# Kernel tuning notes

Hardware: AMD Instinct MI355X
Metric: run time of the kernel (lower is better)

## Reference

```python
import jax, jax.numpy as jnp
import numpy as np

B_POINTS = 2097152
N_LEVELS = 16
BASE_RES = 16.0
PER_LEVEL_SCALE = 1.3195079565048218
MAX_PARAMS = 2 ** 19
PRIMES = np.array([1, 2654435761, 805459861], dtype=np.uint32)
# corner bit pattern: idx in [0,8), dim d offset = (idx >> d) & 1
CORNER_BITS = np.array([[(idx >> d) & 1 for d in range(3)] for idx in range(8)], dtype=np.uint32)  # (8,3)


def _level_meta():
    offsets, sizes, indicators = [], [], []
    off = 0
    for i in range(N_LEVELS):
        res = int(np.ceil(BASE_RES * np.exp(i * np.log(PER_LEVEL_SCALE)) - 1.0)) + 1
        p = res ** 3
        p = p if p % 8 == 0 else ((p + 7) // 8) * 8
        p = min(MAX_PARAMS, p)
        offsets.append(off)
        sizes.append(p)
        indicators.append(1 if res ** 3 <= p else 0)
        off += p
    return offsets, sizes, indicators, off

OFFSETS, MAP_SIZES, INDICATORS, TOTAL_HASH = _level_meta()
TOTAL_PARAMS = TOTAL_HASH * 2  # 2 features per entry, interleaved


def setup_inputs() -> dict:
    key = jax.random.key(0)
    k1, k2 = jax.random.split(key)
    positions = jax.random.uniform(k1, (B_POINTS, 3), dtype=jnp.float32)
    # matches random_initialize: uniform in (-1e-4, 1e-4)
    table = (jax.random.uniform(k2, (TOTAL_PARAMS,), dtype=jnp.float32) * 2.0 - 1.0) * 1e-4
    return {"positions": positions, "table": table}


def _encode(positions, table):
    outs = []
    frac_bits = CORNER_BITS.astype(np.float32)[None, :, :]  # (1,8,3)
    for level in range(N_LEVELS):
        scale = np.float32(BASE_RES * np.exp(level * np.log(PER_LEVEL_SCALE)) - 1.0)
        resolution = np.uint32(np.ceil(scale)) + np.uint32(1)
        pos = positions * scale + 0.5                       # (B,3)
        pos_floor = jnp.floor(pos)
        frac = pos - pos_floor                              # (B,3)
        pg = pos_floor.astype(jnp.uint32)                   # (B,3)
        coords = pg[:, None, :] + CORNER_BITS[None, :, :]   # (B,8,3) uint32
        # trilinear weights per corner
        w = jnp.prod(frac[:, None, :] * frac_bits + (1.0 - frac[:, None, :]) * (1.0 - frac_bits), axis=-1)  # (B,8)
        if INDICATORS[level] == 1:
            s1 = resolution
            s2 = resolution * resolution  # uint32 wraparound safe (res small here)
            h = coords[..., 0] + coords[..., 1] * s1 + coords[..., 2] * s2
        else:
            h = (coords[..., 0] * PRIMES[0]) ^ (coords[..., 1] * PRIMES[1]) ^ (coords[..., 2] * PRIMES[2])
        idx = (h % np.uint32(MAP_SIZES[level])).astype(jnp.int32)
        base = OFFSETS[level] * 2 + idx * 2                 # (B,8) int32
        f0 = jnp.take(table, base)                          # (B,8)
        f1 = jnp.take(table, base + 1)
        outs.append(jnp.stack([jnp.sum(w * f0, axis=-1), jnp.sum(w * f1, axis=-1)], axis=-1))  # (B,2)
    return jnp.concatenate(outs, axis=-1)                   # (B,32)


def reference(positions, table):
    return _encode(positions, table)
```

## Files before the change

### kernel.cpp

```cpp
#include <hip/hip_runtime.h>
#include <cmath>

#define NLEV 16
#define TPB 256

typedef float v4f __attribute__((ext_vector_type(4)));
typedef float v2f __attribute__((ext_vector_type(2)));

static constexpr unsigned kRes[NLEV] = {16u,22u,28u,37u,49u,65u,85u,112u,148u,195u,257u,338u,446u,589u,777u,1025u};
static constexpr unsigned kMsz[NLEV] = {4096u,10648u,21952u,50656u,117656u,274632u,
  524288u,524288u,524288u,524288u,524288u,524288u,524288u,524288u,524288u,524288u};
static constexpr unsigned kOff[NLEV] = {0u,4096u,14744u,36696u,87352u,205008u,479640u,1003928u,
  1528216u,2052504u,2576792u,3101080u,3625368u,4149656u,4673944u,5198232u};
static constexpr int kDense[NLEV] = {1,1,1,1,1,1,0,0,0,0,0,0,0,0,0,0};

struct ScaleParams { float s[NLEV]; };


__device__ __forceinline__ void load_pos(const float* __restrict__ pos, float* sp,
                                         int tid, size_t pbase,
                                         float& px, float& py, float& pz) {
  const float* src = pos + pbase * 3;
  sp[tid]       = __builtin_nontemporal_load(src + tid);
  sp[tid + 256] = __builtin_nontemporal_load(src + tid + 256);
  sp[tid + 512] = __builtin_nontemporal_load(src + tid + 512);
  __syncthreads();
  px = sp[tid*3 + 0]; py = sp[tid*3 + 1]; pz = sp[tid*3 + 2];
}

template<int L>
__global__ __launch_bounds__(TPB, 8) void hash_level(
    const float* __restrict__ pos, const float* __restrict__ table,
    float* __restrict__ ws, float scale, int npts)
{
  __shared__ float sp[TPB * 3];
  const int tid = threadIdx.x;
  const size_t pbase = (size_t)blockIdx.x * TPB;
  float px, py, pz;
  load_pos(pos, sp, tid, pbase, px, py, pz);

  const float x = px * scale + 0.5f;
  const float y = py * scale + 0.5f;
  const float z = pz * scale + 0.5f;
  const float xf = floorf(x), yf = floorf(y), zf = floorf(z);
  const float tx = x - xf, ty = y - yf, tz = z - zf;
  const unsigned xi = (unsigned)xf, yi = (unsigned)yf, zi = (unsigned)zf;

  const unsigned hx[2] = {xi, xi + 1u};
  const unsigned hy[2] = {yi * 2654435761u, (yi + 1u) * 2654435761u};
  const unsigned hz[2] = {zi * 805459861u,  (zi + 1u) * 805459861u};
  const float wx[2] = {1.0f - tx, tx};
  const float wy[2] = {1.0f - ty, ty};
  const float wz[2] = {1.0f - tz, tz};

  const float2* __restrict__ tab2 = (const float2*)table;
  float a0 = 0.0f, a1 = 0.0f;
#pragma unroll
  for (int c = 0; c < 8; ++c) {
    const unsigned idx = (hx[c & 1] ^ hy[(c >> 1) & 1] ^ hz[(c >> 2) & 1]) & (kMsz[L] - 1u);
    const float2 f = tab2[kOff[L] + idx];
    const float w = wx[c & 1] * wy[(c >> 1) & 1] * wz[(c >> 2) & 1];
    a0 = fmaf(w, f.x, a0);
    a1 = fmaf(w, f.y, a1);
  }
  v2f r; r.x = a0; r.y = a1;
  __builtin_nontemporal_store(r, (v2f*)ws + (size_t)L * npts + pbase + tid);
}

__global__ __launch_bounds__(TPB, 4) void dense_levels(
    const float* __restrict__ pos, const float* __restrict__ table,
    float* __restrict__ ws, ScaleParams spar, int npts)
{
  __shared__ float sp[TPB * 3];
  const int tid = threadIdx.x;
  const size_t pbase = (size_t)blockIdx.x * TPB;
  float px, py, pz;
  load_pos(pos, sp, tid, pbase, px, py, pz);

  const float2* __restrict__ tab2 = (const float2*)table;
#pragma unroll
  for (int L = 0; L < 6; ++L) {
    const float scale = spar.s[L];
    const float x = px * scale + 0.5f;
    const float y = py * scale + 0.5f;
    const float z = pz * scale + 0.5f;
    const float xf = floorf(x), yf = floorf(y), zf = floorf(z);
    const float tx = x - xf, ty = y - yf, tz = z - zf;
    const unsigned xi = (unsigned)xf, yi = (unsigned)yf, zi = (unsigned)zf;

    const unsigned r = kRes[L];
    const unsigned hx[2] = {xi, xi + 1u};
    const unsigned hy[2] = {yi * r, (yi + 1u) * r};
    const unsigned hz[2] = {zi * r * r, (zi + 1u) * r * r};
    const float wx[2] = {1.0f - tx, tx};
    const float wy[2] = {1.0f - ty, ty};
    const float wz[2] = {1.0f - tz, tz};

    float a0 = 0.0f, a1 = 0.0f;
#pragma unroll
    for (int c = 0; c < 8; ++c) {
      const unsigned h = hx[c & 1] + hy[(c >> 1) & 1] + hz[(c >> 2) & 1];
      const unsigned idx = (h >= kMsz[L]) ? (h - kMsz[L]) : h;
      const float2 f = tab2[kOff[L] + idx];
      const float w = wx[c & 1] * wy[(c >> 1) & 1] * wz[(c >> 2) & 1];
      a0 = fmaf(w, f.x, a0);
      a1 = fmaf(w, f.y, a1);
    }
    v2f rr; rr.x = a0; rr.y = a1;
    __builtin_nontemporal_store(rr, (v2f*)ws + (size_t)L * npts + pbase + tid);
  }
}

__global__ __launch_bounds__(TPB, 4) void transpose_out(
    const float* __restrict__ ws, float* __restrict__ out, int npts)
{
  __shared__ float lds[TPB * 33];
  const int tid = threadIdx.x;
  const size_t pbase = (size_t)blockIdx.x * TPB;
#pragma unroll
  for (int L = 0; L < NLEV; ++L) {
    const v2f w = __builtin_nontemporal_load((const v2f*)ws + (size_t)L * npts + pbase + tid);
    lds[tid * 33 + 2 * L]     = w.x;
    lds[tid * 33 + 2 * L + 1] = w.y;
  }
  __syncthreads();
  v4f* out4 = (v4f*)out + (size_t)blockIdx.x * (TPB * 32 / 4);
#pragma unroll
  for (int k = 0; k < 8; ++k) {
    const int q  = tid + k * TPB;
    const int p  = q >> 3;
    const int c4 = (q & 7) * 4;
    v4f v;
    v.x = lds[p * 33 + c4 + 0];
    v.y = lds[p * 33 + c4 + 1];
    v.z = lds[p * 33 + c4 + 2];
    v.w = lds[p * 33 + c4 + 3];
    __builtin_nontemporal_store(v, out4 + q);
  }
}

__global__ __launch_bounds__(TPB) void hashenc_kernel(
    const float* __restrict__ pos, const float* __restrict__ table,
    float* __restrict__ out, ScaleParams spar)
{
  __shared__ float lds[TPB * 33];
  const int tid = threadIdx.x;
  const size_t pbase = (size_t)blockIdx.x * TPB;
  {
    const float* src = pos + pbase * 3;
    lds[tid]        = src[tid];
    lds[tid + 256]  = src[tid + 256];
    lds[tid + 512]  = src[tid + 512];
  }
  __syncthreads();
  const float px = lds[tid*3 + 0];
  const float py = lds[tid*3 + 1];
  const float pz = lds[tid*3 + 2];
  __syncthreads();

  const float2* __restrict__ tab2 = (const float2*)table;
  float acc[2 * NLEV];

#pragma unroll
  for (int L = 0; L < NLEV; ++L) {
    const float scale = spar.s[L];
    const float x = px * scale + 0.5f;
    const float y = py * scale + 0.5f;
    const float z = pz * scale + 0.5f;
    const float xf = floorf(x), yf = floorf(y), zf = floorf(z);
    const float tx = x - xf, ty = y - yf, tz = z - zf;
    const unsigned xi = (unsigned)xf, yi = (unsigned)yf, zi = (unsigned)zf;

    unsigned hx[2], hy[2], hz[2];
    if (kDense[L]) {
      const unsigned r = kRes[L];
      hx[0] = xi;          hx[1] = xi + 1u;
      hy[0] = yi * r;      hy[1] = (yi + 1u) * r;
      hz[0] = zi * r * r;  hz[1] = (zi + 1u) * r * r;
    } else {
      hx[0] = xi;                 hx[1] = xi + 1u;
      hy[0] = yi * 2654435761u;   hy[1] = (yi + 1u) * 2654435761u;
      hz[0] = zi * 805459861u;    hz[1] = (zi + 1u) * 805459861u;
    }
    const float wx[2] = {1.0f - tx, tx};
    const float wy[2] = {1.0f - ty, ty};
    const float wz[2] = {1.0f - tz, tz};

    float a0 = 0.0f, a1 = 0.0f;
#pragma unroll
    for (int c = 0; c < 8; ++c) {
      unsigned idx;
      if (kDense[L]) {
        unsigned h = hx[c & 1] + hy[(c >> 1) & 1] + hz[(c >> 2) & 1];
        idx = (h >= kMsz[L]) ? (h - kMsz[L]) : h;
      } else {
        idx = (hx[c & 1] ^ hy[(c >> 1) & 1] ^ hz[(c >> 2) & 1]) & (kMsz[L] - 1u);
      }
      const float2 f = tab2[kOff[L] + idx];
      const float w = wx[c & 1] * wy[(c >> 1) & 1] * wz[(c >> 2) & 1];
      a0 = fmaf(w, f.x, a0);
      a1 = fmaf(w, f.y, a1);
    }
    acc[2 * L]     = a0;
    acc[2 * L + 1] = a1;
  }

#pragma unroll
  for (int c = 0; c < 32; ++c) lds[tid * 33 + c] = acc[c];
  __syncthreads();

  v4f* out4 = (v4f*)out + (size_t)blockIdx.x * (TPB * 32 / 4);
#pragma unroll
  for (int k = 0; k < 8; ++k) {
    const int q  = tid + k * TPB;
    const int p  = q >> 3;
    const int c4 = (q & 7) * 4;
    v4f v;
    v.x = lds[p * 33 + c4 + 0];
    v.y = lds[p * 33 + c4 + 1];
    v.z = lds[p * 33 + c4 + 2];
    v.w = lds[p * 33 + c4 + 3];
    __builtin_nontemporal_store(v, out4 + q);
  }
}

extern "C" void kernel_launch(void* const* d_in, const int* in_sizes, int n_in,
                              void* d_out, int out_size, void* d_ws, size_t ws_size,
                              hipStream_t stream) {
  const float* pos   = (const float*)d_in[0];
  const float* table = (const float*)d_in[1];
  float* out = (float*)d_out;

  ScaleParams sp;
  for (int i = 0; i < NLEV; ++i)
    sp.s[i] = (float)(16.0 * exp((double)i * log(1.3195079565048218)) - 1.0);

  const int npts = in_sizes[0] / 3;
  const int nblk = npts / TPB;
  const size_t need = (size_t)npts * 32 * sizeof(float);

  if (ws_size >= need) {
    float* wsf = (float*)d_ws;
    dense_levels<<<nblk, TPB, 0, stream>>>(pos, table, wsf, sp, npts);
    hash_level< 6><<<nblk, TPB, 0, stream>>>(pos, table, wsf, sp.s[ 6], npts);
    hash_level< 7><<<nblk, TPB, 0, stream>>>(pos, table, wsf, sp.s[ 7], npts);
    hash_level< 8><<<nblk, TPB, 0, stream>>>(pos, table, wsf, sp.s[ 8], npts);
    hash_level< 9><<<nblk, TPB, 0, stream>>>(pos, table, wsf, sp.s[ 9], npts);
    hash_level<10><<<nblk, TPB, 0, stream>>>(pos, table, wsf, sp.s[10], npts);
    hash_level<11><<<nblk, TPB, 0, stream>>>(pos, table, wsf, sp.s[11], npts);
    hash_level<12><<<nblk, TPB, 0, stream>>>(pos, table, wsf, sp.s[12], npts);
    hash_level<13><<<nblk, TPB, 0, stream>>>(pos, table, wsf, sp.s[13], npts);
    hash_level<14><<<nblk, TPB, 0, stream>>>(pos, table, wsf, sp.s[14], npts);
    hash_level<15><<<nblk, TPB, 0, stream>>>(pos, table, wsf, sp.s[15], npts);
    transpose_out<<<nblk, TPB, 0, stream>>>(wsf, out, npts);
  } else {
    hashenc_kernel<<<nblk, TPB, 0, stream>>>(pos, table, out, sp);
  }
}
```

Before: 1.069 ms.

## Fuse hash-level launches into one kernel, two points per thread, paired dense loads

The ten per-level hash kernels become a single `hash_fused` launch. Each block derives its level from the high bits of its block index, so blocks stay grouped by level and each level's table slice keeps its cache locality. Both the dense and hash kernels now handle two points per thread and write 16-byte results. The dense levels fetch the two x-adjacent corners with one 16-byte load, patching the single case where the second corner wraps to the start of the level's table. This trades launch overhead and load-instruction count for more registers per thread, and adds a fallback to the old kernel when the point count is not a power-of-two multiple of 512.

Result: slower. 1.112 ms (+4.0%).

```diff
diff --git a/kernel.cpp b/kernel.cpp
--- a/kernel.cpp
+++ b/kernel.cpp
@@ -16,29 +16,30 @@
 
 struct ScaleParams { float s[NLEV]; };
 
-
-__device__ __forceinline__ void load_pos(const float* __restrict__ pos, float* sp,
-                                         int tid, size_t pbase,
-                                         float& px, float& py, float& pz) {
+__device__ __forceinline__ v4f load4_a8(const float* p) {
+  const float* q = (const float*)__builtin_assume_aligned((const void*)p, 8);
+  v4f v;
+  __builtin_memcpy(&v, q, 16);
+  return v;
+}
+
+__device__ __forceinline__ void load_pos2(const float* __restrict__ pos, float* sp,
+                                          int tid, size_t pbase,
+                                          float& px0, float& py0, float& pz0,
+                                          float& px1, float& py1, float& pz1) {
   const float* src = pos + pbase * 3;
-  sp[tid]       = __builtin_nontemporal_load(src + tid);
-  sp[tid + 256] = __builtin_nontemporal_load(src + tid + 256);
-  sp[tid + 512] = __builtin_nontemporal_load(src + tid + 512);
-  __syncthreads();
-  px = sp[tid*3 + 0]; py = sp[tid*3 + 1]; pz = sp[tid*3 + 2];
-}
-
-template<int L>
-__global__ __launch_bounds__(TPB, 8) void hash_level(
-    const float* __restrict__ pos, const float* __restrict__ table,
-    float* __restrict__ ws, float scale, int npts)
-{
-  __shared__ float sp[TPB * 3];
-  const int tid = threadIdx.x;
-  const size_t pbase = (size_t)blockIdx.x * TPB;
-  float px, py, pz;
-  load_pos(pos, sp, tid, pbase, px, py, pz);
-
+#pragma unroll
+  for (int k = 0; k < 6; ++k)
+    sp[tid + k * TPB] = __builtin_nontemporal_load(src + tid + k * TPB);
+  __syncthreads();
+  px0 = sp[tid * 6 + 0]; py0 = sp[tid * 6 + 1]; pz0 = sp[tid * 6 + 2];
+  px1 = sp[tid * 6 + 3]; py1 = sp[tid * 6 + 4]; pz1 = sp[tid * 6 + 5];
+}
+
+__device__ __forceinline__ v2f dense_point(const float2* __restrict__ tab2,
+                                           float px, float py, float pz,
+                                           float scale, unsigned r, unsigned msz,
+                                           unsigned off) {
   const float x = px * scale + 0.5f;
   const float y = py * scale + 0.5f;
   const float z = pz * scale + 0.5f;
@@ -46,6 +47,45 @@
   const float tx = x - xf, ty = y - yf, tz = z - zf;
   const unsigned xi = (unsigned)xf, yi = (unsigned)yf, zi = (unsigned)zf;
 
+  const unsigned hy[2] = {yi * r, (yi + 1u) * r};
+  const unsigned hz[2] = {zi * r * r, (zi + 1u) * r * r};
+  const float wx0 = 1.0f - tx, wx1 = tx;
+  const float wy[2] = {1.0f - ty, ty};
+  const float wz[2] = {1.0f - tz, tz};
+
+  const float2 g = tab2[off];
+
+  float a0 = 0.0f, a1 = 0.0f;
+#pragma unroll
+  for (int c = 0; c < 4; ++c) {
+    const unsigned h = xi + hy[c & 1] + hz[c >> 1];
+    const unsigned idx = (h >= msz) ? (h - msz) : h;
+    v4f f = load4_a8((const float*)(tab2 + (off + idx)));
+    const bool wrap = (idx == msz - 1u);
+    f.z = wrap ? g.x : f.z;
+    f.w = wrap ? g.y : f.w;
+    const float wyv = wy[c & 1], wzv = wz[c >> 1];
+    const float w0 = (wx0 * wyv) * wzv;
+    const float w1 = (wx1 * wyv) * wzv;
+    a0 = fmaf(w0, f.x, a0);
+    a1 = fmaf(w0, f.y, a1);
+    a0 = fmaf(w1, f.z, a0);
+    a1 = fmaf(w1, f.w, a1);
+  }
+  v2f rr; rr.x = a0; rr.y = a1;
+  return rr;
+}
+
+__device__ __forceinline__ v2f hash_point(const float2* __restrict__ tab2,
+                                          float px, float py, float pz,
+                                          float scale, unsigned off) {
+  const float x = px * scale + 0.5f;
+  const float y = py * scale + 0.5f;
+  const float z = pz * scale + 0.5f;
+  const float xf = floorf(x), yf = floorf(y), zf = floorf(z);
+  const float tx = x - xf, ty = y - yf, tz = z - zf;
+  const unsigned xi = (unsigned)xf, yi = (unsigned)yf, zi = (unsigned)zf;
+
   const unsigned hx[2] = {xi, xi + 1u};
   const unsigned hy[2] = {yi * 2654435761u, (yi + 1u) * 2654435761u};
   const unsigned hz[2] = {zi * 805459861u,  (zi + 1u) * 805459861u};
@@ -53,62 +93,63 @@
   const float wy[2] = {1.0f - ty, ty};
   const float wz[2] = {1.0f - tz, tz};
 
-  const float2* __restrict__ tab2 = (const float2*)table;
   float a0 = 0.0f, a1 = 0.0f;
 #pragma unroll
   for (int c = 0; c < 8; ++c) {
-    const unsigned idx = (hx[c & 1] ^ hy[(c >> 1) & 1] ^ hz[(c >> 2) & 1]) & (kMsz[L] - 1u);
-    const float2 f = tab2[kOff[L] + idx];
+    const unsigned idx = (hx[c & 1] ^ hy[(c >> 1) & 1] ^ hz[(c >> 2) & 1]) & 524287u;
+    const float2 f = tab2[off + idx];
     const float w = wx[c & 1] * wy[(c >> 1) & 1] * wz[(c >> 2) & 1];
     a0 = fmaf(w, f.x, a0);
     a1 = fmaf(w, f.y, a1);
   }
-  v2f r; r.x = a0; r.y = a1;
-  __builtin_nontemporal_store(r, (v2f*)ws + (size_t)L * npts + pbase + tid);
-}
-
-__global__ __launch_bounds__(TPB, 4) void dense_levels(
+  v2f rr; rr.x = a0; rr.y = a1;
+  return rr;
+}
+
+
+__global__ __launch_bounds__(TPB, 4) void dense_levels2(
     const float* __restrict__ pos, const float* __restrict__ table,
     float* __restrict__ ws, ScaleParams spar, int npts)
 {
-  __shared__ float sp[TPB * 3];
-  const int tid = threadIdx.x;
-  const size_t pbase = (size_t)blockIdx.x * TPB;
-  float px, py, pz;
-  load_pos(pos, sp, tid, pbase, px, py, pz);
+  __shared__ float sp[TPB * 6];
+  const int tid = threadIdx.x;
+  const size_t pbase = (size_t)blockIdx.x * (TPB * 2);
+  float px0, py0, pz0, px1, py1, pz1;
+  load_pos2(pos, sp, tid, pbase, px0, py0, pz0, px1, py1, pz1);
 
   const float2* __restrict__ tab2 = (const float2*)table;
 #pragma unroll
   for (int L = 0; L < 6; ++L) {
-    const float scale = spar.s[L];
-    const float x = px * scale + 0.5f;
-    const float y = py * scale + 0.5f;
-    const float z = pz * scale + 0.5f;
-    const float xf = floorf(x), yf = floorf(y), zf = floorf(z);
-    const float tx = x - xf, ty = y - yf, tz = z - zf;
-    const unsigned xi = (unsigned)xf, yi = (unsigned)yf, zi = (unsigned)zf;
-
-    const unsigned r = kRes[L];
-    const unsigned hx[2] = {xi, xi + 1u};
-    const unsigned hy[2] = {yi * r, (yi + 1u) * r};
-    const unsigned hz[2] = {zi * r * r, (zi + 1u) * r * r};
-    const float wx[2] = {1.0f - tx, tx};
-    const float wy[2] = {1.0f - ty, ty};
-    const float wz[2] = {1.0f - tz, tz};
-
-    float a0 = 0.0f, a1 = 0.0f;
-#pragma unroll
-    for (int c = 0; c < 8; ++c) {
-      const unsigned h = hx[c & 1] + hy[(c >> 1) & 1] + hz[(c >> 2) & 1];
-      const unsigned idx = (h >= kMsz[L]) ? (h - kMsz[L]) : h;
-      const float2 f = tab2[kOff[L] + idx];
-      const float w = wx[c & 1] * wy[(c >> 1) & 1] * wz[(c >> 2) & 1];
-      a0 = fmaf(w, f.x, a0);
-      a1 = fmaf(w, f.y, a1);
-    }
-    v2f rr; rr.x = a0; rr.y = a1;
-    __builtin_nontemporal_store(rr, (v2f*)ws + (size_t)L * npts + pbase + tid);
-  }
+    const v2f r0 = dense_point(tab2, px0, py0, pz0, spar.s[L], kRes[L], kMsz[L], kOff[L]);
+    const v2f r1 = dense_point(tab2, px1, py1, pz1, spar.s[L], kRes[L], kMsz[L], kOff[L]);
+    v4f v; v.x = r0.x; v.y = r0.y; v.z = r1.x; v.w = r1.y;
+    __builtin_nontemporal_store(v, (v4f*)ws + ((size_t)L * npts + pbase) / 2 + tid);
+  }
+}
+
+__global__ __launch_bounds__(TPB, 4) void hash_fused(
+    const float* __restrict__ pos, const float* __restrict__ table,
+    float* __restrict__ ws, ScaleParams spar, int lvlShift, int npts)
+{
+  __shared__ float sp[TPB * 6];
+  const int tid = threadIdx.x;
+  const int lvl = 6 + (int)(blockIdx.x >> lvlShift);
+  const unsigned pb = blockIdx.x & ((1u << lvlShift) - 1u);
+
+  float scale = 0.0f;
+#pragma unroll
+  for (int l = 6; l < NLEV; ++l) if (l == lvl) scale = spar.s[l];
+  const unsigned off = kOff[6] + (unsigned)(lvl - 6) * 524288u;
+
+  const size_t pbase = (size_t)pb * (TPB * 2);
+  float px0, py0, pz0, px1, py1, pz1;
+  load_pos2(pos, sp, tid, pbase, px0, py0, pz0, px1, py1, pz1);
+
+  const float2* __restrict__ tab2 = (const float2*)table;
+  const v2f r0 = hash_point(tab2, px0, py0, pz0, scale, off);
+  const v2f r1 = hash_point(tab2, px1, py1, pz1, scale, off);
+  v4f v; v.x = r0.x; v.y = r0.y; v.z = r1.x; v.w = r1.y;
+  __builtin_nontemporal_store(v, (v4f*)ws + ((size_t)lvl * npts + pbase) / 2 + tid);
 }
 
 __global__ __launch_bounds__(TPB, 4) void transpose_out(
@@ -236,24 +277,18 @@
     sp.s[i] = (float)(16.0 * exp((double)i * log(1.3195079565048218)) - 1.0);
 
   const int npts = in_sizes[0] / 3;
-  const int nblk = npts / TPB;
   const size_t need = (size_t)npts * 32 * sizeof(float);
 
-  if (ws_size >= need) {
+  const int npair = npts / (TPB * 2);
+  int sh = 0; while ((1 << sh) < npair) ++sh;
+  const bool ok = (npts % (TPB * 2) == 0) && ((1 << sh) == npair);
+
+  if (ws_size >= need && ok) {
     float* wsf = (float*)d_ws;
-    dense_levels<<<nblk, TPB, 0, stream>>>(pos, table, wsf, sp, npts);
-    hash_level< 6><<<nblk, TPB, 0, stream>>>(pos, table, wsf, sp.s[ 6], npts);
-    hash_level< 7><<<nblk, TPB, 0, stream>>>(pos, table, wsf, sp.s[ 7], npts);
-    hash_level< 8><<<nblk, TPB, 0, stream>>>(pos, table, wsf, sp.s[ 8], npts);
-    hash_level< 9><<<nblk, TPB, 0, stream>>>(pos, table, wsf, sp.s[ 9], npts);
-    hash_level<10><<<nblk, TPB, 0, stream>>>(pos, table, wsf, sp.s[10], npts);
-    hash_level<11><<<nblk, TPB, 0, stream>>>(pos, table, wsf, sp.s[11], npts);
-    hash_level<12><<<nblk, TPB, 0, stream>>>(pos, table, wsf, sp.s[12], npts);
-    hash_level<13><<<nblk, TPB, 0, stream>>>(pos, table, wsf, sp.s[13], npts);
-    hash_level<14><<<nblk, TPB, 0, stream>>>(pos, table, wsf, sp.s[14], npts);
-    hash_level<15><<<nblk, TPB, 0, stream>>>(pos, table, wsf, sp.s[15], npts);
-    transpose_out<<<nblk, TPB, 0, stream>>>(wsf, out, npts);
+    dense_levels2<<<npair, TPB, 0, stream>>>(pos, table, wsf, sp, npts);
+    hash_fused<<<npair * 10, TPB, 0, stream>>>(pos, table, wsf, sp, sh, npts);
+    transpose_out<<<npts / TPB, TPB, 0, stream>>>(wsf, out, npts);
   } else {
-    hashenc_kernel<<<nblk, TPB, 0, stream>>>(pos, table, out, sp);
-  }
-}
+    hashenc_kernel<<<npts / TPB, TPB, 0, stream>>>(pos, table, out, sp);
+  }
+}
```

## Fuse ten hash-level launches into one grid with four points per thread

Applied to the files above, without the earlier changes.

Replaces the ten per-level hash kernels with a single launch whose block index encodes the level, ordered level-major so each level's table region stays cache-resident. Each thread now handles four points and issues all 32 gathers before any arithmetic, with a scheduling barrier, to raise memory-level parallelism. Stores become 16-byte vectors. This removes launch gaps and tail effects between levels, at the cost of higher register pressure and lower occupancy.

Result: no change. 1.073 ms (+0.4%).

```diff
diff --git a/kernel.cpp b/kernel.cpp
--- a/kernel.cpp
+++ b/kernel.cpp
@@ -26,45 +26,6 @@
   sp[tid + 512] = __builtin_nontemporal_load(src + tid + 512);
   __syncthreads();
   px = sp[tid*3 + 0]; py = sp[tid*3 + 1]; pz = sp[tid*3 + 2];
-}
-
-template<int L>
-__global__ __launch_bounds__(TPB, 8) void hash_level(
-    const float* __restrict__ pos, const float* __restrict__ table,
-    float* __restrict__ ws, float scale, int npts)
-{
-  __shared__ float sp[TPB * 3];
-  const int tid = threadIdx.x;
-  const size_t pbase = (size_t)blockIdx.x * TPB;
-  float px, py, pz;
-  load_pos(pos, sp, tid, pbase, px, py, pz);
-
-  const float x = px * scale + 0.5f;
-  const float y = py * scale + 0.5f;
-  const float z = pz * scale + 0.5f;
-  const float xf = floorf(x), yf = floorf(y), zf = floorf(z);
-  const float tx = x - xf, ty = y - yf, tz = z - zf;
-  const unsigned xi = (unsigned)xf, yi = (unsigned)yf, zi = (unsigned)zf;
-
-  const unsigned hx[2] = {xi, xi + 1u};
-  const unsigned hy[2] = {yi * 2654435761u, (yi + 1u) * 2654435761u};
-  const unsigned hz[2] = {zi * 805459861u,  (zi + 1u) * 805459861u};
-  const float wx[2] = {1.0f - tx, tx};
-  const float wy[2] = {1.0f - ty, ty};
-  const float wz[2] = {1.0f - tz, tz};
-
-  const float2* __restrict__ tab2 = (const float2*)table;
-  float a0 = 0.0f, a1 = 0.0f;
-#pragma unroll
-  for (int c = 0; c < 8; ++c) {
-    const unsigned idx = (hx[c & 1] ^ hy[(c >> 1) & 1] ^ hz[(c >> 2) & 1]) & (kMsz[L] - 1u);
-    const float2 f = tab2[kOff[L] + idx];
-    const float w = wx[c & 1] * wy[(c >> 1) & 1] * wz[(c >> 2) & 1];
-    a0 = fmaf(w, f.x, a0);
-    a1 = fmaf(w, f.y, a1);
-  }
-  v2f r; r.x = a0; r.y = a1;
-  __builtin_nontemporal_store(r, (v2f*)ws + (size_t)L * npts + pbase + tid);
 }
 
 __global__ __launch_bounds__(TPB, 4) void dense_levels(
@@ -109,6 +70,87 @@
     v2f rr; rr.x = a0; rr.y = a1;
     __builtin_nontemporal_store(rr, (v2f*)ws + (size_t)L * npts + pbase + tid);
   }
+}
+
+
+__global__ __launch_bounds__(TPB, 4) void hash_fused4(
+    const float* __restrict__ pos, const float* __restrict__ table,
+    float* __restrict__ ws, ScaleParams spar, int lvlShift, int npts)
+{
+  __shared__ float sp[TPB * 12];
+  const int tid = threadIdx.x;
+  const int lvl = 6 + (int)(blockIdx.x >> lvlShift);
+  const unsigned pb = blockIdx.x & ((1u << lvlShift) - 1u);
+
+  float scale = 0.0f;
+#pragma unroll
+  for (int l = 6; l < NLEV; ++l) if (l == lvl) scale = spar.s[l];
+  const unsigned off = kOff[6] + (unsigned)(lvl - 6) * 524288u;
+
+  const size_t pbase = (size_t)pb * (TPB * 4);
+  {
+    const float* src = pos + pbase * 3;
+#pragma unroll
+    for (int k = 0; k < 12; ++k)
+      sp[tid + k * TPB] = __builtin_nontemporal_load(src + tid + k * TPB);
+    __syncthreads();
+  }
+
+  float frac[4][3];
+  unsigned idx[4][8];
+#pragma unroll
+  for (int p = 0; p < 4; ++p) {
+    const float x = sp[tid*12 + p*3 + 0] * scale + 0.5f;
+    const float y = sp[tid*12 + p*3 + 1] * scale + 0.5f;
+    const float z = sp[tid*12 + p*3 + 2] * scale + 0.5f;
+    const float xf = floorf(x), yf = floorf(y), zf = floorf(z);
+    frac[p][0] = x - xf; frac[p][1] = y - yf; frac[p][2] = z - zf;
+    const unsigned xi = (unsigned)xf, yi = (unsigned)yf, zi = (unsigned)zf;
+    const unsigned hx[2] = {xi, xi + 1u};
+    const unsigned hy[2] = {yi * 2654435761u, (yi + 1u) * 2654435761u};
+    const unsigned hz[2] = {zi * 805459861u,  (zi + 1u) * 805459861u};
+#pragma unroll
+    for (int c = 0; c < 8; ++c)
+      idx[p][c] = (hx[c & 1] ^ hy[(c >> 1) & 1] ^ hz[(c >> 2) & 1]) & 524287u;
+  }
+
+  const v2f* __restrict__ t2 = (const v2f*)table + off;
+  v2f f[4][8];
+#pragma unroll
+  for (int p = 0; p < 4; ++p)
+#pragma unroll
+    for (int c = 0; c < 8; ++c)
+      f[p][c] = t2[idx[p][c]];
+  __builtin_amdgcn_sched_barrier(0);
+
+  float w[4][8];
+#pragma unroll
+  for (int p = 0; p < 4; ++p) {
+    const float wx[2] = {1.0f - frac[p][0], frac[p][0]};
+    const float wy[2] = {1.0f - frac[p][1], frac[p][1]};
+    const float wz[2] = {1.0f - frac[p][2], frac[p][2]};
+#pragma unroll
+    for (int c = 0; c < 8; ++c)
+      w[p][c] = wx[c & 1] * wy[(c >> 1) & 1] * wz[(c >> 2) & 1];
+  }
+
+  float acc[4][2];
+#pragma unroll
+  for (int p = 0; p < 4; ++p) {
+    float a0 = 0.0f, a1 = 0.0f;
+#pragma unroll
+    for (int c = 0; c < 8; ++c) {
+      a0 = fmaf(w[p][c], f[p][c].x, a0);
+      a1 = fmaf(w[p][c], f[p][c].y, a1);
+    }
+    acc[p][0] = a0; acc[p][1] = a1;
+  }
+
+  v4f* dst = (v4f*)ws + ((size_t)lvl * npts + pbase) / 2 + 2 * tid;
+  v4f v0; v0.x = acc[0][0]; v0.y = acc[0][1]; v0.z = acc[1][0]; v0.w = acc[1][1];
+  v4f v1; v1.x = acc[2][0]; v1.y = acc[2][1]; v1.z = acc[3][0]; v1.w = acc[3][1];
+  __builtin_nontemporal_store(v0, dst);
+  __builtin_nontemporal_store(v1, dst + 1);
 }
 
 __global__ __launch_bounds__(TPB, 4) void transpose_out(
@@ -236,24 +278,18 @@
     sp.s[i] = (float)(16.0 * exp((double)i * log(1.3195079565048218)) - 1.0);
 
   const int npts = in_sizes[0] / 3;
-  const int nblk = npts / TPB;
   const size_t need = (size_t)npts * 32 * sizeof(float);
 
-  if (ws_size >= need) {
+  const int nq = npts / (TPB * 4);
+  int sh = 0; while ((1 << sh) < nq) ++sh;
+  const bool ok = (npts % (TPB * 4) == 0) && ((1 << sh) == nq);
+
+  if (ws_size >= need && ok) {
     float* wsf = (float*)d_ws;
-    dense_levels<<<nblk, TPB, 0, stream>>>(pos, table, wsf, sp, npts);
-    hash_level< 6><<<nblk, TPB, 0, stream>>>(pos, table, wsf, sp.s[ 6], npts);
-    hash_level< 7><<<nblk, TPB, 0, stream>>>(pos, table, wsf, sp.s[ 7], npts);
-    hash_level< 8><<<nblk, TPB, 0, stream>>>(pos, table, wsf, sp.s[ 8], npts);
-    hash_level< 9><<<nblk, TPB, 0, stream>>>(pos, table, wsf, sp.s[ 9], npts);
-    hash_level<10><<<nblk, TPB, 0, stream>>>(pos, table, wsf, sp.s[10], npts);
-    hash_level<11><<<nblk, TPB, 0, stream>>>(pos, table, wsf, sp.s[11], npts);
-    hash_level<12><<<nblk, TPB, 0, stream>>>(pos, table, wsf, sp.s[12], npts);
-    hash_level<13><<<nblk, TPB, 0, stream>>>(pos, table, wsf, sp.s[13], npts);
-    hash_level<14><<<nblk, TPB, 0, stream>>>(pos, table, wsf, sp.s[14], npts);
-    hash_level<15><<<nblk, TPB, 0, stream>>>(pos, table, wsf, sp.s[15], npts);
-    transpose_out<<<nblk, TPB, 0, stream>>>(wsf, out, npts);
+    dense_levels<<<npts / TPB, TPB, 0, stream>>>(pos, table, wsf, sp, npts);
+    hash_fused4<<<nq * 10, TPB, 0, stream>>>(pos, table, wsf, sp, sh, npts);
+    transpose_out<<<npts / TPB, TPB, 0, stream>>>(wsf, out, npts);
   } else {
-    hashenc_kernel<<<nblk, TPB, 0, stream>>>(pos, table, out, sp);
-  }
-}
+    hashenc_kernel<<<npts / TPB, TPB, 0, stream>>>(pos, table, out, sp);
+  }
+}
```
